# Optimization experiments

Hardware: AMD Instinct MI355X
Metric: run time of the kernel (lower is better)

The kernel has to match this reference:

```python
import jax, jax.numpy as jnp
import numpy as np

B, T, D, H = 2, 2048, 1024, 16
DK = D // H  # 64, head dim (even, required by RoPE pairing)


def setup_inputs() -> dict:
    key = jax.random.key(0)
    ks = jax.random.split(key, 9)
    sc = 1.0 / np.sqrt(D)
    x = jax.random.normal(ks[0], (B, T, D), jnp.float32)
    wq = jax.random.normal(ks[1], (D, D), jnp.float32) * sc
    bq = jax.random.normal(ks[2], (D,), jnp.float32) * 0.01
    wk = jax.random.normal(ks[3], (D, D), jnp.float32) * sc
    bk = jax.random.normal(ks[4], (D,), jnp.float32) * 0.01
    wv = jax.random.normal(ks[5], (D, D), jnp.float32) * sc
    bv = jax.random.normal(ks[6], (D,), jnp.float32) * 0.01
    wo = jax.random.normal(ks[7], (D, D), jnp.float32) * sc
    bo = jax.random.normal(ks[8], (D,), jnp.float32) * 0.01
    # causal mask, True = masked (matches masked_fill semantics); dim==3 -> broadcast over heads
    attn_mask = jnp.triu(jnp.ones((T, T), dtype=bool), 1)[None]  # [1,T,T]
    return dict(x=x, wq=wq, bq=bq, wk=wk, bk=bk, wv=wv, bv=bv, wo=wo, bo=bo,
                attn_mask=attn_mask)


def _rope(xh, sin, cos):
    # xh: [B,H,T,DK]; sin/cos: [T,DK/2]
    x1 = xh[..., 0::2]
    x2 = xh[..., 1::2]
    return jnp.stack([x1 * cos - x2 * sin, x1 * sin + x2 * cos], axis=-1).reshape(xh.shape)


def reference(x, wq, bq, wk, bk, wv, bv, wo, bo, attn_mask):
    q = (x @ wq.T + bq).reshape(B, T, H, DK).transpose(0, 2, 1, 3)  # [B,H,T,DK]
    k = (x @ wk.T + bk).reshape(B, T, H, DK).transpose(0, 2, 1, 3)
    v = (x @ wv.T + bv).reshape(B, T, H, DK).transpose(0, 2, 1, 3)
    # RoPE (seq_offset = 0)
    theta = 10000.0 ** (jnp.arange(0, DK, 2, dtype=jnp.float32) / DK)  # [DK/2]
    pos = jnp.arange(T, dtype=jnp.float32)[:, None]                    # [T,1]
    ang = pos / theta                                                  # [T,DK/2]
    sin, cos = jnp.sin(ang), jnp.cos(ang)
    q = _rope(q, sin, cos)
    k = _rope(k, sin, cos)
    # fp32 stable attention (inputs already fp32)
    scores = jnp.einsum('bhtd,bhsd->bhts', q, k) / np.sqrt(DK)
    scores = jnp.where(attn_mask[:, None], -1e9, scores)  # mask broadcast over heads
    attn = jax.nn.softmax(scores, axis=-1)
    ctx = jnp.einsum('bhts,bhsd->bhtd', attn, v)
    ctx = ctx.transpose(0, 2, 1, 3).reshape(B, T, D)
    return ctx @ wo.T + bo
```

## Files before the change

### kernel.cpp

```cpp
#include <hip/hip_runtime.h>
#include <stdint.h>
#include <stddef.h>

#define T_ 2048
#define D_ 1024
#define H_ 16

typedef __attribute__((ext_vector_type(8))) short short8;
typedef __attribute__((ext_vector_type(4))) float f32x4;
typedef __attribute__((ext_vector_type(4))) short s16x4;

__device__ __forceinline__ unsigned short f2bf(float f){
  union { float f; unsigned u; } c; c.f = f;
  unsigned u = c.u;
  return (unsigned short)((u + 0x7fffu + ((u >> 16) & 1u)) >> 16);
}

__device__ __forceinline__ unsigned pk_bf16(float lo, float hi){
  unsigned r;
  asm("v_cvt_pk_bf16_f32 %0, %1, %2" : "=v"(r) : "v"(lo), "v"(hi));
  return r;
}

__device__ __forceinline__ float fexp2(float x){
#if __has_builtin(__builtin_amdgcn_exp2f)
  return __builtin_amdgcn_exp2f(x);
#else
  return exp2f(x);
#endif
}

__device__ __forceinline__ f32x4 mfma16(short8 a, short8 b, f32x4 c){
  return __builtin_amdgcn_mfma_f32_16x16x32_bf16(a, b, c, 0, 0, 0);
}

__device__ __forceinline__ void gload16(const void* g, void* l){
  __builtin_amdgcn_global_load_lds(
      (const __attribute__((address_space(1))) unsigned*)g,
      (__attribute__((address_space(3))) unsigned*)l, 16, 0, 0);
}

__global__ __launch_bounds__(256) void k_prep(const float* __restrict__ x,
    const float* __restrict__ wq, const float* __restrict__ wk,
    const float* __restrict__ wv, const float* __restrict__ wo,
    unsigned short* __restrict__ xb, unsigned short* __restrict__ wqkv,
    unsigned short* __restrict__ wob, float* __restrict__ tab)
{
  if (blockIdx.x < 256){
    int i = blockIdx.x * 256 + threadIdx.x;
    int t = i >> 5, p = i & 31;
    float ang = (float)t * powf(10000.0f, -(float)p * (1.0f / 32.0f));
    tab[i] = sinf(ang);
    tab[T_ * 32 + i] = cosf(ang);
  }
  const long long NX = 4194304LL, NW = 1048576LL;
  long long base = ((long long)blockIdx.x * 256 + threadIdx.x) * 8;
  const float* s; unsigned short* d;
  if (base < NX){ s = x + base; d = xb + base; }
  else if (base < NX + 3*NW){
    long long j = base - NX;
    if (j < NW) s = wq + j;
    else if (j < 2*NW) s = wk + (j - NW);
    else s = wv + (j - 2*NW);
    d = wqkv + j;
  } else if (base < NX + 4*NW){
    long long j = base - NX - 3*NW;
    s = wo + j; d = wob + j;
  } else return;
  float4 a = *(const float4*)s;
  float4 b = *(const float4*)(s + 4);
  union { unsigned u[4]; short8 v; } o;
  o.u[0] = pk_bf16(a.x, a.y);
  o.u[1] = pk_bf16(a.z, a.w);
  o.u[2] = pk_bf16(b.x, b.y);
  o.u[3] = pk_bf16(b.z, b.w);
  *(short8*)d = o.v;
}

__device__ __forceinline__ void gemm_core(const unsigned short* __restrict__ A,
    const unsigned short* __restrict__ Bm, int m0, int n0,
    unsigned short* lA0, unsigned short* lB0,
    unsigned short* lA1, unsigned short* lB1, f32x4 (&acc)[4][4])
{
  const int tid = threadIdx.x, lane = tid & 63, wave = tid >> 6;
  const int wr = wave >> 1, wc = wave & 1;
  for (int mi = 0; mi < 4; ++mi)
    for (int ni = 0; ni < 4; ++ni)
      acc[mi][ni] = (f32x4){0.f, 0.f, 0.f, 0.f};

  auto STAGE = [&](int k0, unsigned short* lA, unsigned short* lB){
#pragma unroll
    for (int p = 0; p < 4; ++p){
      int c = p * 256 + tid, r = c >> 3, s = c & 7;
      int gs = (s ^ (r & 7)) << 3;
      gload16(A + (size_t)(m0 + r) * 1024 + k0 + gs, lA + c * 8);
      gload16(Bm + (size_t)(n0 + r) * 1024 + k0 + gs, lB + c * 8);
    }
  };
  auto COMPUTE = [&](const unsigned short* lA, const unsigned short* lB){
#pragma unroll
    for (int kk = 0; kk < 2; ++kk){
      int kslot = kk * 4 + (lane >> 4);
      short8 af[4], bf[4];
#pragma unroll
      for (int mi = 0; mi < 4; ++mi){
        int row = wr * 64 + mi * 16 + (lane & 15);
        af[mi] = *(const short8*)(lA + row * 64 + ((kslot ^ (row & 7)) << 3));
      }
#pragma unroll
      for (int ni = 0; ni < 4; ++ni){
        int row = wc * 64 + ni * 16 + (lane & 15);
        bf[ni] = *(const short8*)(lB + row * 64 + ((kslot ^ (row & 7)) << 3));
      }
#pragma unroll
      for (int mi = 0; mi < 4; ++mi)
#pragma unroll
        for (int ni = 0; ni < 4; ++ni)
          acc[mi][ni] = mfma16(af[mi], bf[ni], acc[mi][ni]);
    }
  };

  STAGE(0, lA0, lB0);
  asm volatile("s_waitcnt vmcnt(0)" ::: "memory");
  __builtin_amdgcn_s_barrier();
  for (int k0 = 0; k0 < 1024; k0 += 64){
    bool ev = !((k0 >> 6) & 1);
    if (k0 + 64 < 1024)
      STAGE(k0 + 64, ev ? lA1 : lA0, ev ? lB1 : lB0);
    COMPUTE(ev ? lA0 : lA1, ev ? lB0 : lB1);
    asm volatile("s_waitcnt vmcnt(0)" ::: "memory");
    __builtin_amdgcn_s_barrier();
  }
}

__global__ __launch_bounds__(256) void k_qkv(const unsigned short* __restrict__ xb,
    const unsigned short* __restrict__ wqkv,
    const float* __restrict__ bq, const float* __restrict__ bk, const float* __restrict__ bv,
    const float* __restrict__ tab,
    unsigned short* __restrict__ Qw, unsigned short* __restrict__ Kw,
    unsigned short* __restrict__ Vw)
{
  __shared__ alignas(16) unsigned short lA0[128 * 64];
  __shared__ alignas(16) unsigned short lB0[128 * 64];
  __shared__ alignas(16) unsigned short lA1[128 * 64];
  __shared__ alignas(16) unsigned short lB1[128 * 64];
  int m0 = blockIdx.y * 128, n0 = blockIdx.x * 128;
  f32x4 acc[4][4];
  gemm_core(xb, wqkv, m0, n0, lA0, lB0, lA1, lB1, acc);
  int lane = threadIdx.x & 63, wave = threadIdx.x >> 6;
  int wr = wave >> 1, wc = wave & 1;
  int mat = n0 >> 10;
  const float* bias = (mat == 0) ? bq : (mat == 1 ? bk : bv);
  const float* st = tab; const float* ct = tab + T_ * 32;
  if (mat < 2){
    unsigned short* Out = (mat == 0) ? Qw : Kw;
    float qs = (mat == 0) ? 0.18033688011116f : 1.0f;
    for (int mi = 0; mi < 4; ++mi){
      for (int ni = 0; ni < 4; ++ni){
        int col = n0 + wc * 64 + ni * 16 + (lane & 15);
        int nn = col & 1023, h = nn >> 6, dd = nn & 63;
        float bsv = bias[nn];
        f32x4 v4 = acc[mi][ni];
#pragma unroll
        for (int r = 0; r < 4; ++r){
          int m = m0 + wr * 64 + mi * 16 + ((lane >> 4) << 2) + r;
          int bb = m >> 11, t = m & 2047;
          float v = v4[r] + bsv;
          float u = __shfl_xor(v, 1);
          int p = dd >> 1;
          float sv = st[t * 32 + p], cv = ct[t * 32 + p];
          float res = (dd & 1) ? (u * sv + v * cv) : (v * cv - u * sv);
          Out[((size_t)(bb * H_ + h) * T_ + t) * 64 + dd] = f2bf(res * qs);
        }
      }
    }
  } else {
    for (int mi = 0; mi < 4; ++mi){
      for (int ni = 0; ni < 4; ++ni){
        int col = n0 + wc * 64 + ni * 16 + (lane & 15);
        int nn = col & 1023, h = nn >> 6, dd = nn & 63;
        float bsv = bias[nn];
        int mb = m0 + wr * 64 + mi * 16 + ((lane >> 4) << 2);
        int bb = mb >> 11, t = mb & 2047;
        f32x4 v4 = acc[mi][ni];
        s16x4 o;
#pragma unroll
        for (int r = 0; r < 4; ++r) o[r] = (short)f2bf(v4[r] + bsv);
        *(s16x4*)(Vw + ((size_t)((bb * H_ + h) * 64 + dd)) * T_ + t) = o;
      }
    }
  }
}

__global__ __launch_bounds__(256) void k_attn(const unsigned short* __restrict__ Qw,
    const unsigned short* __restrict__ Kw, const unsigned short* __restrict__ Vt_g,
    unsigned short* __restrict__ ctxb)
{
  __shared__ alignas(16) unsigned short Kl0[128 * 64];
  __shared__ alignas(16) unsigned short Vl0[64 * 128];
  __shared__ alignas(16) unsigned short Kl1[128 * 64];
  __shared__ alignas(16) unsigned short Vl1[64 * 128];
  int qt = (int)gridDim.y - 1 - (int)blockIdx.y;
  int bh = blockIdx.x;
  int tid = threadIdx.x, lane = tid & 63, wave = tid >> 6;
  const unsigned short* Qb = Qw + (size_t)bh * T_ * 64;
  const unsigned short* Kb = Kw + (size_t)bh * T_ * 64;
  const unsigned short* Vb = Vt_g + (size_t)bh * 64 * T_;
  int q0 = qt * 128 + wave * 32;

  short8 qf[2][2];
#pragma unroll
  for (int mi = 0; mi < 2; ++mi){
    const unsigned short* qp = Qb + (size_t)(q0 + mi * 16 + (lane & 15)) * 64 + ((lane >> 4) << 3);
    qf[mi][0] = *(const short8*)qp;
    qf[mi][1] = *(const short8*)(qp + 32);
  }
  float mr[2] = {-1e30f, -1e30f}, lr[2] = {0.f, 0.f};
  f32x4 acc_o[2][4];
#pragma unroll
  for (int mi = 0; mi < 2; ++mi)
#pragma unroll
    for (int df = 0; df < 4; ++df) acc_o[mi][df] = (f32x4){0.f, 0.f, 0.f, 0.f};

  const int src0 = ((lane >> 4) & 1) * 32 + (lane & 15);
  const int src1 = src0 + 16;
  const bool hiHalf = lane >= 32;

  auto STAGE = [&](int j0, unsigned short* Kd, unsigned short* Vd){
#pragma unroll
    for (int p = 0; p < 4; ++p){
      int c = p * 256 + tid, r = c >> 3, s = c & 7;
      gload16(Kb + (size_t)(j0 + r) * 64 + ((s ^ (r & 7)) << 3), Kd + c * 8);
    }
#pragma unroll
    for (int p = 0; p < 4; ++p){
      int c = p * 256 + tid, r = c >> 4, s = c & 15;
      gload16(Vb + (size_t)r * T_ + j0 + ((s ^ (r & 7)) << 3), Vd + c * 8);
    }
  };

  auto COMPUTE = [&](int j0, const unsigned short* Kc, const unsigned short* Vc){
    bool need_mask = (j0 + 127 > q0);
    f32x4 accs[2][8];
#pragma unroll
    for (int mi = 0; mi < 2; ++mi)
#pragma unroll
      for (int jf = 0; jf < 8; ++jf) accs[mi][jf] = (f32x4){0.f, 0.f, 0.f, 0.f};
#pragma unroll
    for (int kk = 0; kk < 2; ++kk){
      int kslot = kk * 4 + (lane >> 4);
      short8 kf[8];
#pragma unroll
      for (int jf = 0; jf < 8; ++jf){
        int row = jf * 16 + (lane & 15);
        kf[jf] = *(const short8*)(Kc + row * 64 + ((kslot ^ (row & 7)) << 3));
      }
#pragma unroll
      for (int mi = 0; mi < 2; ++mi)
#pragma unroll
        for (int jf = 0; jf < 8; ++jf)
          accs[mi][jf] = mfma16(kf[jf], qf[mi][kk], accs[mi][jf]);
    }

    unsigned w0[2][8], w1[2][8];
#pragma unroll
    for (int mi = 0; mi < 2; ++mi){
      int qa = q0 + mi * 16 + (lane & 15);
      float mx = -1e30f;
#pragma unroll
      for (int jf = 0; jf < 8; ++jf)
#pragma unroll
        for (int r = 0; r < 4; ++r){
          float sv = accs[mi][jf][r];
          if (need_mask){
            int ja = j0 + jf * 16 + ((lane >> 4) << 2) + r;
            if (ja > qa) sv = -1e30f;
          }
          accs[mi][jf][r] = sv;
          mx = fmaxf(mx, sv);
        }
      mx = fmaxf(mx, __shfl_xor(mx, 16));
      mx = fmaxf(mx, __shfl_xor(mx, 32));
      float mn = fmaxf(mr[mi], mx);
      float sc = fexp2(mr[mi] - mn);
      mr[mi] = mn;
      float rs = 0.f;
#pragma unroll
      for (int jf = 0; jf < 8; ++jf)
#pragma unroll
        for (int r = 0; r < 4; ++r){
          float pe = fexp2(accs[mi][jf][r] - mn);
          accs[mi][jf][r] = pe;
          rs += pe;
        }
      rs += __shfl_xor(rs, 16);
      rs += __shfl_xor(rs, 32);
      lr[mi] = lr[mi] * sc + rs;
#pragma unroll
      for (int df = 0; df < 4; ++df){
        f32x4 a = acc_o[mi][df];
        a[0] *= sc; a[1] *= sc; a[2] *= sc; a[3] *= sc;
        acc_o[mi][df] = a;
      }
#pragma unroll
      for (int jf = 0; jf < 8; ++jf){
        w0[mi][jf] = pk_bf16(accs[mi][jf][0], accs[mi][jf][1]);
        w1[mi][jf] = pk_bf16(accs[mi][jf][2], accs[mi][jf][3]);
      }
    }

#pragma unroll
    for (int kk = 0; kk < 4; ++kk){
      int jslot = kk * 4 + (lane >> 4);
      short8 vf[4];
#pragma unroll
      for (int df = 0; df < 4; ++df){
        int row = df * 16 + (lane & 15);
        vf[df] = *(const short8*)(Vc + row * 128 + ((jslot ^ (row & 7)) << 3));
      }
#pragma unroll
      for (int mi = 0; mi < 2; ++mi){
        unsigned lo0 = (unsigned)__shfl((int)w0[mi][2*kk],   src0);
        unsigned hi0 = (unsigned)__shfl((int)w0[mi][2*kk+1], src0);
        unsigned lo1 = (unsigned)__shfl((int)w1[mi][2*kk],   src0);
        unsigned hi1 = (unsigned)__shfl((int)w1[mi][2*kk+1], src0);
        unsigned lo2 = (unsigned)__shfl((int)w0[mi][2*kk],   src1);
        unsigned hi2 = (unsigned)__shfl((int)w0[mi][2*kk+1], src1);
        unsigned lo3 = (unsigned)__shfl((int)w1[mi][2*kk],   src1);
        unsigned hi3 = (unsigned)__shfl((int)w1[mi][2*kk+1], src1);
        union { unsigned u[4]; short8 v; } pb;
        pb.u[0] = hiHalf ? hi0 : lo0;
        pb.u[1] = hiHalf ? hi1 : lo1;
        pb.u[2] = hiHalf ? hi2 : lo2;
        pb.u[3] = hiHalf ? hi3 : lo3;
#pragma unroll
        for (int df = 0; df < 4; ++df)
          acc_o[mi][df] = mfma16(vf[df], pb.v, acc_o[mi][df]);
      }
    }
  };

  int ntiles = qt + 1;
  STAGE(0, Kl0, Vl0);
  asm volatile("s_waitcnt vmcnt(0)" ::: "memory");
  __builtin_amdgcn_s_barrier();
  for (int jt = 0; jt < ntiles; ++jt){
    bool ev = !(jt & 1);
    unsigned short* Kc = ev ? Kl0 : Kl1;
    unsigned short* Vc = ev ? Vl0 : Vl1;
    if (jt + 1 < ntiles)
      STAGE((jt + 1) * 128, ev ? Kl1 : Kl0, ev ? Vl1 : Vl0);
    if (jt * 128 <= q0 + 31)
      COMPUTE(jt * 128, Kc, Vc);
    asm volatile("s_waitcnt vmcnt(0)" ::: "memory");
    __builtin_amdgcn_s_barrier();
  }

  int bb = bh >> 4, h = bh & 15;
#pragma unroll
  for (int mi = 0; mi < 2; ++mi){
    float inv = 1.0f / lr[mi];
    int t = q0 + mi * 16 + (lane & 15);
#pragma unroll
    for (int df = 0; df < 4; ++df){
      int d0 = df * 16 + ((lane >> 4) << 2);
      f32x4 a = acc_o[mi][df];
      s16x4 o;
#pragma unroll
      for (int r = 0; r < 4; ++r) o[r] = (short)f2bf(a[r] * inv);
      *(s16x4*)(ctxb + ((size_t)(bb * T_ + t)) * 1024 + h * 64 + d0) = o;
    }
  }
}

__global__ __launch_bounds__(256) void k_oproj(const unsigned short* __restrict__ ctxb,
    const unsigned short* __restrict__ wob, const float* __restrict__ bo,
    float* __restrict__ out)
{
  __shared__ alignas(16) unsigned short lA0[128 * 64];
  __shared__ alignas(16) unsigned short lB0[128 * 64];
  __shared__ alignas(16) unsigned short lA1[128 * 64];
  __shared__ alignas(16) unsigned short lB1[128 * 64];
  int m0 = blockIdx.y * 128, n0 = blockIdx.x * 128;
  f32x4 acc[4][4];
  gemm_core(ctxb, wob, m0, n0, lA0, lB0, lA1, lB1, acc);
  int lane = threadIdx.x & 63, wave = threadIdx.x >> 6;
  int wr = wave >> 1, wc = wave & 1;
  for (int mi = 0; mi < 4; ++mi)
    for (int ni = 0; ni < 4; ++ni){
      int col = n0 + wc * 64 + ni * 16 + (lane & 15);
      float bsv = bo[col];
      f32x4 v4 = acc[mi][ni];
#pragma unroll
      for (int r = 0; r < 4; ++r){
        int m = m0 + wr * 64 + mi * 16 + ((lane >> 4) << 2) + r;
        out[(size_t)m * 1024 + col] = v4[r] + bsv;
      }
    }
}

extern "C" void kernel_launch(void* const* d_in, const int* in_sizes, int n_in,
                              void* d_out, int out_size, void* d_ws, size_t ws_size,
                              hipStream_t stream)
{
  const float* x  = (const float*)d_in[0];
  const float* wq = (const float*)d_in[1];
  const float* bq = (const float*)d_in[2];
  const float* wk = (const float*)d_in[3];
  const float* bk = (const float*)d_in[4];
  const float* wv = (const float*)d_in[5];
  const float* bv = (const float*)d_in[6];
  const float* wo = (const float*)d_in[7];
  const float* bo = (const float*)d_in[8];
  char* w = (char*)d_ws;
  unsigned short* xb   = (unsigned short*)(w);
  unsigned short* wqkv = (unsigned short*)(w + (8 << 20));
  unsigned short* wob  = (unsigned short*)(w + (14 << 20));
  unsigned short* Qw   = (unsigned short*)(w + (16 << 20));
  unsigned short* Kw   = (unsigned short*)(w + (24 << 20));
  unsigned short* Vw   = (unsigned short*)(w + (32 << 20));
  unsigned short* ctxb = (unsigned short*)(w + (40 << 20));
  float* tab           = (float*)(w + (48 << 20));

  k_prep<<<4096, 256, 0, stream>>>(x, wq, wk, wv, wo, xb, wqkv, wob, tab);
  k_qkv<<<dim3(24, 32), 256, 0, stream>>>(xb, wqkv, bq, bk, bv, tab, Qw, Kw, Vw);
  k_attn<<<dim3(32, 16), 256, 0, stream>>>(Qw, Kw, Vw, ctxb);
  k_oproj<<<dim3(8, 32), 256, 0, stream>>>(ctxb, wob, bo, (float*)d_out);
}
```

Before: 130.0 us.

## Pair high and low causal query tiles per attention block for load balance

Each attention block now runs 8 waves (512 threads) and handles two 128-row query tiles, one from the top and one from the bottom of the causal triangle, with each wave owning 16 rows from each tile. The grid shrinks to 8 blocks in y, and each block streams K/V up to the larger tile while skipping MFMA work for the tile that is already finished. The aim is to even out per-block work under the causal mask and share K/V staging across two query tiles. The cost is that waves working on the low tile go idle on later iterations, and the larger block lowers register headroom.

```diff
diff --git a/kernel.cpp b/kernel.cpp
--- a/kernel.cpp
+++ b/kernel.cpp
@@ -192,7 +192,7 @@
   }
 }
 
-__global__ __launch_bounds__(256) void k_attn(const unsigned short* __restrict__ Qw,
+__global__ __launch_bounds__(512) void k_attn(const unsigned short* __restrict__ Qw,
     const unsigned short* __restrict__ Kw, const unsigned short* __restrict__ Vt_g,
     unsigned short* __restrict__ ctxb)
 {
@@ -200,18 +200,19 @@
   __shared__ alignas(16) unsigned short Vl0[64 * 128];
   __shared__ alignas(16) unsigned short Kl1[128 * 64];
   __shared__ alignas(16) unsigned short Vl1[64 * 128];
-  int qt = (int)gridDim.y - 1 - (int)blockIdx.y;
   int bh = blockIdx.x;
+  int yy = blockIdx.y;
+  int qtH = 15 - yy, qtL = yy;
   int tid = threadIdx.x, lane = tid & 63, wave = tid >> 6;
   const unsigned short* Qb = Qw + (size_t)bh * T_ * 64;
   const unsigned short* Kb = Kw + (size_t)bh * T_ * 64;
   const unsigned short* Vb = Vt_g + (size_t)bh * 64 * T_;
-  int q0 = qt * 128 + wave * 32;
+  const int qb[2] = { qtH * 128 + wave * 16, qtL * 128 + wave * 16 };
 
   short8 qf[2][2];
 #pragma unroll
   for (int mi = 0; mi < 2; ++mi){
-    const unsigned short* qp = Qb + (size_t)(q0 + mi * 16 + (lane & 15)) * 64 + ((lane >> 4) << 3);
+    const unsigned short* qp = Qb + (size_t)(qb[mi] + (lane & 15)) * 64 + ((lane >> 4) << 3);
     qf[mi][0] = *(const short8*)qp;
     qf[mi][1] = *(const short8*)(qp + 32);
   }
@@ -228,19 +229,18 @@
 
   auto STAGE = [&](int j0, unsigned short* Kd, unsigned short* Vd){
 #pragma unroll
-    for (int p = 0; p < 4; ++p){
-      int c = p * 256 + tid, r = c >> 3, s = c & 7;
-      gload16(Kb + (size_t)(j0 + r) * 64 + ((s ^ (r & 7)) << 3), Kd + c * 8);
-    }
-#pragma unroll
-    for (int p = 0; p < 4; ++p){
-      int c = p * 256 + tid, r = c >> 4, s = c & 15;
-      gload16(Vb + (size_t)r * T_ + j0 + ((s ^ (r & 7)) << 3), Vd + c * 8);
+    for (int p = 0; p < 2; ++p){
+      int c = p * 512 + tid;
+      int rK = c >> 3, sK = c & 7;
+      gload16(Kb + (size_t)(j0 + rK) * 64 + ((sK ^ (rK & 7)) << 3), Kd + c * 8);
+      int rV = c >> 4, sV = c & 15;
+      gload16(Vb + (size_t)rV * T_ + j0 + ((sV ^ (rV & 7)) << 3), Vd + c * 8);
     }
   };
 
   auto COMPUTE = [&](int j0, const unsigned short* Kc, const unsigned short* Vc){
-    bool need_mask = (j0 + 127 > q0);
+    bool act[2] = { j0 <= qb[0] + 15, j0 <= qb[1] + 15 };
+    if (!act[0] && !act[1]) return;
     f32x4 accs[2][8];
 #pragma unroll
     for (int mi = 0; mi < 2; ++mi)
@@ -257,15 +257,18 @@
       }
 #pragma unroll
       for (int mi = 0; mi < 2; ++mi)
-#pragma unroll
-        for (int jf = 0; jf < 8; ++jf)
-          accs[mi][jf] = mfma16(kf[jf], qf[mi][kk], accs[mi][jf]);
+        if (act[mi])
+#pragma unroll
+          for (int jf = 0; jf < 8; ++jf)
+            accs[mi][jf] = mfma16(kf[jf], qf[mi][kk], accs[mi][jf]);
     }
 
     unsigned w0[2][8], w1[2][8];
 #pragma unroll
     for (int mi = 0; mi < 2; ++mi){
-      int qa = q0 + mi * 16 + (lane & 15);
+      if (!act[mi]) continue;
+      int qa = qb[mi] + (lane & 15);
+      bool need_mask = (j0 + 127 > qb[mi]);
       float mx = -1e30f;
 #pragma unroll
       for (int jf = 0; jf < 8; ++jf)
@@ -320,6 +323,7 @@
       }
 #pragma unroll
       for (int mi = 0; mi < 2; ++mi){
+        if (!act[mi]) continue;
         unsigned lo0 = (unsigned)__shfl((int)w0[mi][2*kk],   src0);
         unsigned hi0 = (unsigned)__shfl((int)w0[mi][2*kk+1], src0);
         unsigned lo1 = (unsigned)__shfl((int)w1[mi][2*kk],   src0);
@@ -340,7 +344,7 @@
     }
   };
 
-  int ntiles = qt + 1;
+  int ntiles = qtH + 1;
   STAGE(0, Kl0, Vl0);
   asm volatile("s_waitcnt vmcnt(0)" ::: "memory");
   __builtin_amdgcn_s_barrier();
@@ -350,8 +354,7 @@
     unsigned short* Vc = ev ? Vl0 : Vl1;
     if (jt + 1 < ntiles)
       STAGE((jt + 1) * 128, ev ? Kl1 : Kl0, ev ? Vl1 : Vl0);
-    if (jt * 128 <= q0 + 31)
-      COMPUTE(jt * 128, Kc, Vc);
+    COMPUTE(jt * 128, Kc, Vc);
     asm volatile("s_waitcnt vmcnt(0)" ::: "memory");
     __builtin_amdgcn_s_barrier();
   }
@@ -360,7 +363,7 @@
 #pragma unroll
   for (int mi = 0; mi < 2; ++mi){
     float inv = 1.0f / lr[mi];
-    int t = q0 + mi * 16 + (lane & 15);
+    int t = qb[mi] + (lane & 15);
 #pragma unroll
     for (int df = 0; df < 4; ++df){
       int d0 = df * 16 + ((lane >> 4) << 2);
@@ -424,6 +427,6 @@
 
   k_prep<<<4096, 256, 0, stream>>>(x, wq, wk, wv, wo, xb, wqkv, wob, tab);
   k_qkv<<<dim3(24, 32), 256, 0, stream>>>(xb, wqkv, bq, bk, bv, tab, Qw, Kw, Vw);
-  k_attn<<<dim3(32, 16), 256, 0, stream>>>(Qw, Kw, Vw, ctxb);
+  k_attn<<<dim3(32, 8), 512, 0, stream>>>(Qw, Kw, Vw, ctxb);
   k_oproj<<<dim3(8, 32), 256, 0, stream>>>(ctxb, wob, bo, (float*)d_out);
 }
```

New measurement: 125.4 us. 1.04x faster.
